# Optimization experiments

Hardware: AMD Instinct MI355X
Metric: run time of the kernel (lower is better)

The kernel has to match this reference:

```python
import jax, jax.numpy as jnp
import numpy as np

E = 128      # embedding_dim
H = 64       # hidden_dim
B = 2048     # batch
L = 200      # history length
NEG = -1e30  # stand-in for -inf (avoids NaN for all-pad rows; same math when any key unmasked)


def setup_inputs() -> dict:
    key = jax.random.key(0)
    ks = jax.random.split(key, 10)
    s1 = 1.0 / np.sqrt(4 * E)
    s2 = 1.0 / np.sqrt(H)
    return {
        "query": jax.random.normal(ks[0], (B, E), jnp.float32),
        "keys": jax.random.normal(ks[1], (B, L, E), jnp.float32),
        "mask": jax.random.randint(ks[2], (B, L), 0, 2, jnp.int32),
        "W1": jax.random.uniform(ks[3], (4 * E, H), jnp.float32, -s1, s1),
        "b1": jax.random.uniform(ks[4], (H,), jnp.float32, -s1, s1),
        "W2": jax.random.uniform(ks[5], (H, H), jnp.float32, -s2, s2),
        "b2": jax.random.uniform(ks[6], (H,), jnp.float32, -s2, s2),
        "W3": jax.random.uniform(ks[7], (H, 1), jnp.float32, -s2, s2),
        "b3": jax.random.uniform(ks[8], (1,), jnp.float32, -s2, s2),
        "no_hist": jax.random.normal(ks[9], (E,), jnp.float32) * 0.001,
    }


def reference(query, keys, mask, W1, b1, W2, b2, W3, b3, no_hist):
    # q expanded over L, 4-way concat features: [q, k, q*k, q-k] -> (B, L, 4E)
    q = jnp.broadcast_to(query[:, None, :], keys.shape)
    attn_in = jnp.concatenate([q, keys, q * keys, q - keys], axis=-1)
    # 3-layer MLP scorer -> (B, L)
    h = jax.nn.relu(attn_in @ W1 + b1)
    h = jax.nn.relu(h @ W2 + b2)
    scores = (h @ W3 + b3)[..., 0]
    # masked softmax over L, then zero masked slots and renormalize
    m = mask.astype(scores.dtype)
    scores = jnp.where(m == 0, NEG, scores)
    attn = jax.nn.softmax(scores, axis=1) * m
    denom = jnp.sum(attn, axis=1, keepdims=True)
    attn = attn / (denom + 1e-12)
    # weighted sum of keys -> (B, E)
    user_interest = jnp.einsum("bl,ble->be", attn, keys)
    # rows with no history get the learned no-hist embedding
    all_pad = jnp.sum(m, axis=1) == 0  # (B,)
    user_interest = jnp.where(all_pad[:, None], no_hist[None, :], user_interest)
    return user_interest
```

## Files before the change

kernel.cpp:

```cpp
#include <hip/hip_runtime.h>


#define NB 2048
#define LE 128
#define LH 64
#define LL 200

typedef short bf16x8 __attribute__((ext_vector_type(8)));
typedef float f32x4 __attribute__((ext_vector_type(4)));

__device__ __forceinline__ short f2bf(float f) {
  unsigned u = __float_as_uint(f);
  u += 0x7fffu + ((u >> 16) & 1u);
  return (short)(u >> 16);
}

__device__ __forceinline__ void gll16(const void* g, void* l) {
  __builtin_amdgcn_global_load_lds(
      (const __attribute__((address_space(1))) void*)g,
      (__attribute__((address_space(3))) void*)l, 16, 0, 0);
}

struct __align__(16) SM {
  union {
    float stag[4][2][16 * 128];
    short scratch[64 * 136];
  } u;
  short h1[4][16 * 72];
  float scores[208];
  float q[128];
  float bias1[64];
  float b2s[64];
  float w3s[64];
  float red[16];
};

__global__ void k0_prep(const float* __restrict__ W1, const float* __restrict__ W2,
                        float* __restrict__ BD, float* __restrict__ Cq,
                        float* __restrict__ AD, short* __restrict__ W2T) {
  int idx = blockIdx.x * 256 + threadIdx.x;
  if (idx < 8192) {
    int h = idx >> 7, e = idx & 127;
    BD[idx] = W1[(128 + e) * LH + h] - W1[(384 + e) * LH + h];
    Cq[idx] = W1[(256 + e) * LH + h];
    int e2 = idx >> 6, h2 = idx & 63;
    AD[idx] = W1[e2 * LH + h2] + W1[(384 + e2) * LH + h2];
    if (idx < 4096) {
      int c = idx >> 6, k = idx & 63;
      W2T[idx] = f2bf(W2[k * LH + c]);
    }
  }
}

__global__ void __launch_bounds__(256, 2)
din_attn(const float* __restrict__ query, const float* __restrict__ keysg,
         const int* __restrict__ mask, const float* __restrict__ b1,
         const float* __restrict__ b2, const float* __restrict__ W3,
         const float* __restrict__ no_hist,
         const float* __restrict__ BD, const float* __restrict__ Cq,
         const float* __restrict__ AD, const short* __restrict__ W2T,
         float* __restrict__ out)
{
  __shared__ SM sm;
  const int b    = blockIdx.x;
  const int t    = threadIdx.x;
  const int lane = t & 63;
  const int wv   = t >> 6;
  const int col  = lane & 15;
  const int quad = lane >> 4;
  const int l31  = lane & 31;
  const int lh   = lane >> 5;

  int my_mask = 0;
  if (t < LL) my_mask = mask[b * LL + t];
  if (t < LE) sm.q[t] = query[b * LE + t];
  if (t < LH) { sm.b2s[t] = b2[t]; sm.w3s[t] = W3[t]; }
  __syncthreads();

  bf16x8 fB2[4][2];
  #pragma unroll
  for (int n = 0; n < 4; ++n)
    #pragma unroll
    for (int k2 = 0; k2 < 2; ++k2)
      fB2[n][k2] = *(const bf16x8*)&W2T[(n * 16 + col) * 64 + k2 * 32 + quad * 8];

  short* scratch = &sm.u.scratch[0];
  #pragma unroll
  for (int i = 0; i < 4; ++i) {
    int idx = (t + 256 * i) * 8;
    int h = idx >> 7, e0 = idx & 127;
    float4 bd0 = *(const float4*)&BD[idx];
    float4 bd1 = *(const float4*)&BD[idx + 4];
    float4 c0  = *(const float4*)&Cq[idx];
    float4 c1  = *(const float4*)&Cq[idx + 4];
    bf16x8 w;
    w[0] = f2bf(bd0.x + sm.q[e0 + 0] * c0.x);
    w[1] = f2bf(bd0.y + sm.q[e0 + 1] * c0.y);
    w[2] = f2bf(bd0.z + sm.q[e0 + 2] * c0.z);
    w[3] = f2bf(bd0.w + sm.q[e0 + 3] * c0.w);
    w[4] = f2bf(bd1.x + sm.q[e0 + 4] * c1.x);
    w[5] = f2bf(bd1.y + sm.q[e0 + 5] * c1.y);
    w[6] = f2bf(bd1.z + sm.q[e0 + 6] * c1.z);
    w[7] = f2bf(bd1.w + sm.q[e0 + 7] * c1.w);
    *(bf16x8*)&scratch[h * 136 + e0] = w;
  }
  {
    int h = lane;
    float acc = 0.f;
    #pragma unroll 8
    for (int e = wv * 32; e < wv * 32 + 32; ++e)
      acc = fmaf(sm.q[e], AD[e * LH + h], acc);
    float* biasp = (float*)&sm.h1[0][0];
    biasp[wv * 64 + h] = acc;
  }
  __syncthreads();

  bf16x8 fB1[4][4];
  #pragma unroll
  for (int n = 0; n < 4; ++n)
    #pragma unroll
    for (int kt = 0; kt < 4; ++kt)
      fB1[n][kt] = *(const bf16x8*)&scratch[(n * 16 + col) * 136 + kt * 32 + quad * 8];

  if (t < LH) {
    const float* biasp = (const float*)&sm.h1[0][0];
    sm.bias1[t] = b1[t] + biasp[t] + biasp[64 + t] + biasp[128 + t] + biasp[192 + t];
  }
  __syncthreads();

  const float* kb = keysg + (size_t)b * LL * LE;
  short* h1w = &sm.h1[wv][0];
  const int mts[4] = {wv, wv + 4, wv + 8, 12};
  const int nt = (wv == 0) ? 4 : 3;
  float* stg0 = &sm.u.stag[wv][0][0];
  float* stg1 = &sm.u.stag[wv][1][0];

  auto issue_tile = [&](float* dst, int mt) {
    #pragma unroll
    for (int i = 0; i < 8; ++i) {
      int rl  = 2 * i + lh;
      int row = mt * 16 + rl;
      row = row < LL ? row : LL - 1;
      const float* src = kb + row * LE + ((l31 ^ (rl & 7)) << 2);
      gll16(src, dst + i * 256);
    }
  };

  auto load_frags = [&](const float* sb, bf16x8 (&a)[4]) {
    #pragma unroll
    for (int kt = 0; kt < 4; ++kt) {
      const int b0 = kt * 8 + quad * 2;
      float4 v0 = *(const float4*)&sb[col * 128 + ((b0 ^ (col & 7)) << 2)];
      float4 v1 = *(const float4*)&sb[col * 128 + (((b0 + 1) ^ (col & 7)) << 2)];
      bf16x8 av;
      av[0] = f2bf(v0.x); av[1] = f2bf(v0.y); av[2] = f2bf(v0.z); av[3] = f2bf(v0.w);
      av[4] = f2bf(v1.x); av[5] = f2bf(v1.y); av[6] = f2bf(v1.z); av[7] = f2bf(v1.w);
      a[kt] = av;
    }
  };

  auto compute_tile = [&](const bf16x8 (&a)[4], int mt) {
    #pragma unroll
    for (int n = 0; n < 4; ++n) {
      f32x4 acc = {0.f, 0.f, 0.f, 0.f};
      #pragma unroll
      for (int kt = 0; kt < 4; ++kt)
        acc = __builtin_amdgcn_mfma_f32_16x16x32_bf16(a[kt], fB1[n][kt], acc, 0, 0, 0);
      float bias = sm.bias1[n * 16 + col];
      #pragma unroll
      for (int j = 0; j < 4; ++j)
        h1w[(quad * 4 + j) * 72 + n * 16 + col] = f2bf(fmaxf(acc[j] + bias, 0.f));
    }
    bf16x8 a2[2];
    #pragma unroll
    for (int k2 = 0; k2 < 2; ++k2)
      a2[k2] = *(const bf16x8*)&h1w[col * 72 + k2 * 32 + quad * 8];
    float p[4] = {0.f, 0.f, 0.f, 0.f};
    #pragma unroll
    for (int n = 0; n < 4; ++n) {
      f32x4 c2 = {0.f, 0.f, 0.f, 0.f};
      c2 = __builtin_amdgcn_mfma_f32_16x16x32_bf16(a2[0], fB2[n][0], c2, 0, 0, 0);
      c2 = __builtin_amdgcn_mfma_f32_16x16x32_bf16(a2[1], fB2[n][1], c2, 0, 0, 0);
      float bb = sm.b2s[n * 16 + col];
      float w3 = sm.w3s[n * 16 + col];
      #pragma unroll
      for (int j = 0; j < 4; ++j)
        p[j] = fmaf(fmaxf(c2[j] + bb, 0.f), w3, p[j]);
    }
    #pragma unroll
    for (int j = 0; j < 4; ++j) {
      #pragma unroll
      for (int off = 1; off < 16; off <<= 1)
        p[j] += __shfl_xor(p[j], off);
      if (col == 0) sm.scores[mt * 16 + quad * 4 + j] = p[j];
    }
  };

  issue_tile(stg0, mts[0]);
  issue_tile(stg1, mts[1]);

  bf16x8 ka[4][4];
  #pragma unroll
  for (int i = 0; i < 4; ++i) {
    if (i < nt) {
      if (i < nt - 1) asm volatile("s_waitcnt vmcnt(8)" ::: "memory");
      else            asm volatile("s_waitcnt vmcnt(0)" ::: "memory");
      __builtin_amdgcn_sched_barrier(0);
      load_frags((i & 1) ? stg1 : stg0, ka[i]);
      asm volatile("s_waitcnt lgkmcnt(0)" ::: "memory");
      __builtin_amdgcn_sched_barrier(0);
      if (i + 2 < nt) issue_tile((i & 1) ? stg1 : stg0, mts[i + 2]);
      __builtin_amdgcn_sched_barrier(0);
      compute_tile(ka[i], mts[i]);
    }
  }
  __syncthreads();

  float sc = (t < LL) ? sm.scores[t] : -3.0e38f;
  float vmax = (my_mask != 0) ? sc : -3.0e38f;
  #pragma unroll
  for (int off = 1; off < 64; off <<= 1) vmax = fmaxf(vmax, __shfl_xor(vmax, off));
  if (lane == 0) sm.red[wv] = vmax;
  __syncthreads();
  float M = fmaxf(fmaxf(sm.red[0], sm.red[1]), fmaxf(sm.red[2], sm.red[3]));
  float ex = (t < LL && my_mask != 0) ? __expf(sc - M) : 0.f;
  float vsum = ex;
  #pragma unroll
  for (int off = 1; off < 64; off <<= 1) vsum += __shfl_xor(vsum, off);
  if (lane == 0) sm.red[4 + wv] = vsum;
  __syncthreads();
  float Z = sm.red[4] + sm.red[5] + sm.red[6] + sm.red[7];
  bool allpad = !(Z > 0.f);
  float rz = allpad ? 0.f : (1.f / Z);
  if (t < 208) sm.scores[t] = (t < LL) ? ex * rz : 0.f;
  __syncthreads();

  {
    float aw[4] = {0.f, 0.f, 0.f, 0.f};
    #pragma unroll
    for (int i = 0; i < 4; ++i)
      if (i < nt) aw[i] = sm.scores[mts[i] * 16 + col];

    float* redf = (float*)&sm.h1[0][0];
    #pragma unroll
    for (int kt = 0; kt < 4; ++kt) {
      float s[8] = {0.f, 0.f, 0.f, 0.f, 0.f, 0.f, 0.f, 0.f};
      #pragma unroll
      for (int i = 0; i < 4; ++i) {
        if (i < nt) {
          const int* kv = (const int*)&ka[i][kt];
          #pragma unroll
          for (int w = 0; w < 4; ++w) {
            unsigned u = (unsigned)kv[w];
            s[2 * w]     = fmaf(aw[i], __uint_as_float(u << 16), s[2 * w]);
            s[2 * w + 1] = fmaf(aw[i], __uint_as_float(u & 0xffff0000u), s[2 * w + 1]);
          }
        }
      }
      #pragma unroll
      for (int j = 0; j < 8; ++j) {
        #pragma unroll
        for (int off = 1; off < 16; off <<= 1)
          s[j] += __shfl_xor(s[j], off);
      }
      if (col == 0) {
        #pragma unroll
        for (int j = 0; j < 8; ++j)
          redf[wv * 128 + kt * 32 + quad * 8 + j] = s[j];
      }
    }
    __syncthreads();
    if (t < LE) {
      float s = redf[t] + redf[128 + t] + redf[256 + t] + redf[384 + t];
      if (allpad) s = no_hist[t];
      out[b * LE + t] = s;
    }
  }
}

extern "C" void kernel_launch(void* const* d_in, const int* in_sizes, int n_in,
                              void* d_out, int out_size, void* d_ws, size_t ws_size,
                              hipStream_t stream) {
  (void)in_sizes; (void)n_in; (void)ws_size; (void)out_size;
  const float* query   = (const float*)d_in[0];
  const float* keysg   = (const float*)d_in[1];
  const int*   mask    = (const int*)d_in[2];
  const float* W1      = (const float*)d_in[3];
  const float* b1      = (const float*)d_in[4];
  const float* W2      = (const float*)d_in[5];
  const float* b2      = (const float*)d_in[6];
  const float* W3      = (const float*)d_in[7];
  const float* no_hist = (const float*)d_in[9];

  float* BD  = (float*)d_ws;
  float* Cq  = BD + 8192;
  float* AD  = Cq + 8192;
  short* W2T = (short*)(AD + 8192);

  k0_prep<<<32, 256, 0, stream>>>(W1, W2, BD, Cq, AD, W2T);
  din_attn<<<NB, 256, 0, stream>>>(query, keysg, mask, b1, b2, W3, no_hist,
                                   BD, Cq, AD, W2T, (float*)d_out);
}
```

Before: 328.0 us.

## Keep MLP weight fragments in LDS and load keys directly to raise occupancy

The W1 and W2 MFMA B-fragments now sit in LDS, laid out per lane, and are read inside each tile computation instead of being held in registers. The global_load_lds staging buffers are dropped, and key rows are loaded straight from global memory into registers with a simple software prefetch order. Launch bounds go from 2 to 4 blocks per SM, and the precomputed weights move from the workspace into __device__ globals. This trades extra LDS reads per tile and the loss of the explicit async-copy pipeline for lower register and LDS pressure and higher occupancy to hide memory latency.

```diff
diff --git a/kernel.cpp b/kernel.cpp
--- a/kernel.cpp
+++ b/kernel.cpp
@@ -9,23 +9,35 @@
 typedef short bf16x8 __attribute__((ext_vector_type(8)));
 typedef float f32x4 __attribute__((ext_vector_type(4)));
 
+__device__ float g_BD[8192];
+__device__ float g_Cq[8192];
+__device__ float g_AD[8192];
+__device__ short g_W2T[4096];
+
 __device__ __forceinline__ short f2bf(float f) {
   unsigned u = __float_as_uint(f);
   u += 0x7fffu + ((u >> 16) & 1u);
   return (short)(u >> 16);
 }
 
-__device__ __forceinline__ void gll16(const void* g, void* l) {
-  __builtin_amdgcn_global_load_lds(
-      (const __attribute__((address_space(1))) void*)g,
-      (__attribute__((address_space(3))) void*)l, 16, 0, 0);
+__global__ void k0_prep(const float* __restrict__ W1, const float* __restrict__ W2) {
+  int idx = blockIdx.x * 256 + threadIdx.x;
+  if (idx < 8192) {
+    int h = idx >> 7, e = idx & 127;
+    g_BD[idx] = W1[(128 + e) * LH + h] - W1[(384 + e) * LH + h];
+    g_Cq[idx] = W1[(256 + e) * LH + h];
+    int e2 = idx >> 6, h2 = idx & 63;
+    g_AD[idx] = W1[e2 * LH + h2] + W1[(384 + e2) * LH + h2];
+    if (idx < 4096) {
+      int c = idx >> 6, k = idx & 63;
+      g_W2T[idx] = f2bf(W2[k * LH + c]);
+    }
+  }
 }
 
 struct __align__(16) SM {
-  union {
-    float stag[4][2][16 * 128];
-    short scratch[64 * 136];
-  } u;
+  short flds1[16 * 64 * 8];
+  short flds2[8 * 64 * 8];
   short h1[4][16 * 72];
   float scores[208];
   float q[128];
@@ -35,31 +47,11 @@
   float red[16];
 };
 
-__global__ void k0_prep(const float* __restrict__ W1, const float* __restrict__ W2,
-                        float* __restrict__ BD, float* __restrict__ Cq,
-                        float* __restrict__ AD, short* __restrict__ W2T) {
-  int idx = blockIdx.x * 256 + threadIdx.x;
-  if (idx < 8192) {
-    int h = idx >> 7, e = idx & 127;
-    BD[idx] = W1[(128 + e) * LH + h] - W1[(384 + e) * LH + h];
-    Cq[idx] = W1[(256 + e) * LH + h];
-    int e2 = idx >> 6, h2 = idx & 63;
-    AD[idx] = W1[e2 * LH + h2] + W1[(384 + e2) * LH + h2];
-    if (idx < 4096) {
-      int c = idx >> 6, k = idx & 63;
-      W2T[idx] = f2bf(W2[k * LH + c]);
-    }
-  }
-}
-
-__global__ void __launch_bounds__(256, 2)
+__global__ void __launch_bounds__(256, 4)
 din_attn(const float* __restrict__ query, const float* __restrict__ keysg,
          const int* __restrict__ mask, const float* __restrict__ b1,
          const float* __restrict__ b2, const float* __restrict__ W3,
-         const float* __restrict__ no_hist,
-         const float* __restrict__ BD, const float* __restrict__ Cq,
-         const float* __restrict__ AD, const short* __restrict__ W2T,
-         float* __restrict__ out)
+         const float* __restrict__ no_hist, float* __restrict__ out)
 {
   __shared__ SM sm;
   const int b    = blockIdx.x;
@@ -68,8 +60,6 @@
   const int wv   = t >> 6;
   const int col  = lane & 15;
   const int quad = lane >> 4;
-  const int l31  = lane & 31;
-  const int lh   = lane >> 5;
 
   int my_mask = 0;
   if (t < LL) my_mask = mask[b * LL + t];
@@ -77,22 +67,14 @@
   if (t < LH) { sm.b2s[t] = b2[t]; sm.w3s[t] = W3[t]; }
   __syncthreads();
 
-  bf16x8 fB2[4][2];
-  #pragma unroll
-  for (int n = 0; n < 4; ++n)
-    #pragma unroll
-    for (int k2 = 0; k2 < 2; ++k2)
-      fB2[n][k2] = *(const bf16x8*)&W2T[(n * 16 + col) * 64 + k2 * 32 + quad * 8];
-
-  short* scratch = &sm.u.scratch[0];
   #pragma unroll
   for (int i = 0; i < 4; ++i) {
     int idx = (t + 256 * i) * 8;
     int h = idx >> 7, e0 = idx & 127;
-    float4 bd0 = *(const float4*)&BD[idx];
-    float4 bd1 = *(const float4*)&BD[idx + 4];
-    float4 c0  = *(const float4*)&Cq[idx];
-    float4 c1  = *(const float4*)&Cq[idx + 4];
+    float4 bd0 = *(const float4*)&g_BD[idx];
+    float4 bd1 = *(const float4*)&g_BD[idx + 4];
+    float4 c0  = *(const float4*)&g_Cq[idx];
+    float4 c1  = *(const float4*)&g_Cq[idx + 4];
     bf16x8 w;
     w[0] = f2bf(bd0.x + sm.q[e0 + 0] * c0.x);
     w[1] = f2bf(bd0.y + sm.q[e0 + 1] * c0.y);
@@ -102,25 +84,30 @@
     w[5] = f2bf(bd1.y + sm.q[e0 + 5] * c1.y);
     w[6] = f2bf(bd1.z + sm.q[e0 + 6] * c1.z);
     w[7] = f2bf(bd1.w + sm.q[e0 + 7] * c1.w);
-    *(bf16x8*)&scratch[h * 136 + e0] = w;
+    int n = h >> 4, cc = h & 15, kt = e0 >> 5, qd = (e0 >> 3) & 3;
+    *(bf16x8*)&sm.flds1[(((n * 4 + kt) * 64) + qd * 16 + cc) * 8] = w;
+  }
+  {
+    int l = t & 63, f0 = t >> 6;
+    #pragma unroll
+    for (int ii = 0; ii < 2; ++ii) {
+      int f = f0 + ii * 4;
+      int n = f >> 1, k2 = f & 1;
+      int cc = l & 15, qd = l >> 4;
+      *(bf16x8*)&sm.flds2[(f * 64 + l) * 8] =
+          *(const bf16x8*)&g_W2T[(n * 16 + cc) * 64 + k2 * 32 + qd * 8];
+    }
   }
   {
     int h = lane;
     float acc = 0.f;
     #pragma unroll 8
     for (int e = wv * 32; e < wv * 32 + 32; ++e)
-      acc = fmaf(sm.q[e], AD[e * LH + h], acc);
+      acc = fmaf(sm.q[e], g_AD[e * LH + h], acc);
     float* biasp = (float*)&sm.h1[0][0];
     biasp[wv * 64 + h] = acc;
   }
   __syncthreads();
-
-  bf16x8 fB1[4][4];
-  #pragma unroll
-  for (int n = 0; n < 4; ++n)
-    #pragma unroll
-    for (int kt = 0; kt < 4; ++kt)
-      fB1[n][kt] = *(const bf16x8*)&scratch[(n * 16 + col) * 136 + kt * 32 + quad * 8];
 
   if (t < LH) {
     const float* biasp = (const float*)&sm.h1[0][0];
@@ -131,27 +118,16 @@
   const float* kb = keysg + (size_t)b * LL * LE;
   short* h1w = &sm.h1[wv][0];
   const int mts[4] = {wv, wv + 4, wv + 8, 12};
-  const int nt = (wv == 0) ? 4 : 3;
-  float* stg0 = &sm.u.stag[wv][0][0];
-  float* stg1 = &sm.u.stag[wv][1][0];
-
-  auto issue_tile = [&](float* dst, int mt) {
-    #pragma unroll
-    for (int i = 0; i < 8; ++i) {
-      int rl  = 2 * i + lh;
-      int row = mt * 16 + rl;
-      row = row < LL ? row : LL - 1;
-      const float* src = kb + row * LE + ((l31 ^ (rl & 7)) << 2);
-      gll16(src, dst + i * 256);
-    }
-  };
-
-  auto load_frags = [&](const float* sb, bf16x8 (&a)[4]) {
+  bf16x8 ka[4][4];
+
+  auto load_tile = [&](bf16x8 (&a)[4], int mt) {
+    int row = mt * 16 + col;
+    row = row < LL ? row : LL - 1;
+    const float* rp = kb + row * LE;
     #pragma unroll
     for (int kt = 0; kt < 4; ++kt) {
-      const int b0 = kt * 8 + quad * 2;
-      float4 v0 = *(const float4*)&sb[col * 128 + ((b0 ^ (col & 7)) << 2)];
-      float4 v1 = *(const float4*)&sb[col * 128 + (((b0 + 1) ^ (col & 7)) << 2)];
+      float4 v0 = *(const float4*)&rp[kt * 32 + quad * 8];
+      float4 v1 = *(const float4*)&rp[kt * 32 + quad * 8 + 4];
       bf16x8 av;
       av[0] = f2bf(v0.x); av[1] = f2bf(v0.y); av[2] = f2bf(v0.z); av[3] = f2bf(v0.w);
       av[4] = f2bf(v1.x); av[5] = f2bf(v1.y); av[6] = f2bf(v1.z); av[7] = f2bf(v1.w);
@@ -164,8 +140,10 @@
     for (int n = 0; n < 4; ++n) {
       f32x4 acc = {0.f, 0.f, 0.f, 0.f};
       #pragma unroll
-      for (int kt = 0; kt < 4; ++kt)
-        acc = __builtin_amdgcn_mfma_f32_16x16x32_bf16(a[kt], fB1[n][kt], acc, 0, 0, 0);
+      for (int kt = 0; kt < 4; ++kt) {
+        bf16x8 wf = *(const bf16x8*)&sm.flds1[((n * 4 + kt) * 64 + lane) * 8];
+        acc = __builtin_amdgcn_mfma_f32_16x16x32_bf16(a[kt], wf, acc, 0, 0, 0);
+      }
       float bias = sm.bias1[n * 16 + col];
       #pragma unroll
       for (int j = 0; j < 4; ++j)
@@ -178,9 +156,11 @@
     float p[4] = {0.f, 0.f, 0.f, 0.f};
     #pragma unroll
     for (int n = 0; n < 4; ++n) {
+      bf16x8 w20 = *(const bf16x8*)&sm.flds2[((n * 2 + 0) * 64 + lane) * 8];
+      bf16x8 w21 = *(const bf16x8*)&sm.flds2[((n * 2 + 1) * 64 + lane) * 8];
       f32x4 c2 = {0.f, 0.f, 0.f, 0.f};
-      c2 = __builtin_amdgcn_mfma_f32_16x16x32_bf16(a2[0], fB2[n][0], c2, 0, 0, 0);
-      c2 = __builtin_amdgcn_mfma_f32_16x16x32_bf16(a2[1], fB2[n][1], c2, 0, 0, 0);
+      c2 = __builtin_amdgcn_mfma_f32_16x16x32_bf16(a2[0], w20, c2, 0, 0, 0);
+      c2 = __builtin_amdgcn_mfma_f32_16x16x32_bf16(a2[1], w21, c2, 0, 0, 0);
       float bb = sm.b2s[n * 16 + col];
       float w3 = sm.w3s[n * 16 + col];
       #pragma unroll
@@ -196,24 +176,14 @@
     }
   };
 
-  issue_tile(stg0, mts[0]);
-  issue_tile(stg1, mts[1]);
-
-  bf16x8 ka[4][4];
-  #pragma unroll
-  for (int i = 0; i < 4; ++i) {
-    if (i < nt) {
-      if (i < nt - 1) asm volatile("s_waitcnt vmcnt(8)" ::: "memory");
-      else            asm volatile("s_waitcnt vmcnt(0)" ::: "memory");
-      __builtin_amdgcn_sched_barrier(0);
-      load_frags((i & 1) ? stg1 : stg0, ka[i]);
-      asm volatile("s_waitcnt lgkmcnt(0)" ::: "memory");
-      __builtin_amdgcn_sched_barrier(0);
-      if (i + 2 < nt) issue_tile((i & 1) ? stg1 : stg0, mts[i + 2]);
-      __builtin_amdgcn_sched_barrier(0);
-      compute_tile(ka[i], mts[i]);
-    }
-  }
+  load_tile(ka[0], mts[0]);
+  load_tile(ka[1], mts[1]);
+  compute_tile(ka[0], mts[0]);
+  load_tile(ka[2], mts[2]);
+  compute_tile(ka[1], mts[1]);
+  if (wv == 0) load_tile(ka[3], 12);
+  compute_tile(ka[2], mts[2]);
+  if (wv == 0) compute_tile(ka[3], 12);
   __syncthreads();
 
   float sc = (t < LL) ? sm.scores[t] : -3.0e38f;
@@ -236,6 +206,7 @@
   __syncthreads();
 
   {
+    const int nt = (wv == 0) ? 4 : 3;
     float aw[4] = {0.f, 0.f, 0.f, 0.f};
     #pragma unroll
     for (int i = 0; i < 4; ++i)
@@ -281,7 +252,7 @@
 extern "C" void kernel_launch(void* const* d_in, const int* in_sizes, int n_in,
                               void* d_out, int out_size, void* d_ws, size_t ws_size,
                               hipStream_t stream) {
-  (void)in_sizes; (void)n_in; (void)ws_size; (void)out_size;
+  (void)in_sizes; (void)n_in; (void)ws_size; (void)out_size; (void)d_ws;
   const float* query   = (const float*)d_in[0];
   const float* keysg   = (const float*)d_in[1];
   const int*   mask    = (const int*)d_in[2];
@@ -292,12 +263,7 @@
   const float* W3      = (const float*)d_in[7];
   const float* no_hist = (const float*)d_in[9];
 
-  float* BD  = (float*)d_ws;
-  float* Cq  = BD + 8192;
-  float* AD  = Cq + 8192;
-  short* W2T = (short*)(AD + 8192);
-
-  k0_prep<<<32, 256, 0, stream>>>(W1, W2, BD, Cq, AD, W2T);
+  k0_prep<<<32, 256, 0, stream>>>(W1, W2);
   din_attn<<<NB, 256, 0, stream>>>(query, keysg, mask, b1, b2, W3, no_hist,
-                                   BD, Cq, AD, W2T, (float*)d_out);
-}
+                                   (float*)d_out);
+}
```

Measured after the change: 319.6 us. 1.03x faster.
